# Kernel tuning notes

Measured on AMD Instinct MI355X. Metric: run time of the kernel, lower is better.

Reference implementation:

```python
import jax, jax.numpy as jnp
import numpy as np

DELTA_VAR = 0.5
DELTA_DIST = 1.5
VAR_WEIGHT = 1.0
DIST_WEIGHT = 1.0
REG_WEIGHT = 0.001
K = 16  # number of clusters (labels are in [0, K))


def setup_inputs() -> dict:
    key = jax.random.key(0)
    k1, k2 = jax.random.split(key)
    data = jax.random.normal(k1, (32, 512, 1024), dtype=jnp.float32)
    labels = jax.random.randint(k2, (512, 1024), 0, K, dtype=jnp.int32)
    return {"data": data, "labels": labels}


def reference(data, labels):
    D = data.shape[0]
    pts = data.reshape(D, -1).T          # [N, D] per-pixel embeddings
    lab = labels.reshape(-1)             # [N]

    # Per-cluster size and mean (center). All K clusters are present.
    counts = jax.ops.segment_sum(jnp.ones_like(lab, dtype=pts.dtype), lab,
                                 num_segments=K)          # [K]
    sums = jax.ops.segment_sum(pts, lab, num_segments=K)  # [K, D]
    centers = sums / counts[:, None]                      # [K, D]

    # Variance term: sum over all points of hinge(||center - x|| - dv)^2 / K
    diff = centers[lab] - pts                             # [N, D]
    dist = jnp.sqrt(jnp.sum(diff * diff, axis=-1))        # [N]
    var_term = jnp.sum(jnp.maximum(dist - DELTA_VAR, 0.0) ** 2) / K

    # Distance term: ordered pairs i != j of hinge(2*dd - ||ci - cj||)^2
    cd = centers[:, None, :] - centers[None, :, :]        # [K, K, D]
    sq = jnp.sum(cd * cd, axis=-1)                        # [K, K]
    eye = jnp.eye(K, dtype=bool)
    pd = jnp.sqrt(jnp.where(eye, 1.0, sq))                # safe sqrt on diag
    hinge = jnp.where(eye, 0.0, jnp.maximum(2.0 * DELTA_DIST - pd, 0.0) ** 2)
    dist_term = jnp.sum(hinge) / (K * (K - 1))

    # Regularization term: mean center norm
    reg_term = jnp.sum(jnp.sqrt(jnp.sum(centers * centers, axis=-1))) / K

    return VAR_WEIGHT * var_term + DIST_WEIGHT * dist_term + REG_WEIGHT * reg_term
```

## Files before the change

kernel.cpp:

```cpp
#include <hip/hip_runtime.h>


constexpr int KC = 16;
constexpr int DD = 32;
constexpr int NN = 512 * 1024;
constexpr int N4 = NN / 4;
constexpr int N2 = NN / 2;
constexpr int CHUNKS = 32;
constexpr int GROUPS_PER_CHUNK = N4 / CHUNKS;
constexpr int K1_ITERS = GROUPS_PER_CHUNK / 256;

constexpr int WS_P  = 0;
constexpr int WS_CP = 16384;

__global__ __launch_bounds__(256) void kA_sums(const float4* __restrict__ data4,
                                               const int4* __restrict__ lab4,
                                               float* __restrict__ ws,
                                               float* __restrict__ out) {
    const int tid = threadIdx.x;
    const int chunk = blockIdx.x;
    const int d = blockIdx.y;
    const bool doCnt = (d == 0);

    if (chunk == 0 && d == 0 && tid == 0) out[0] = 0.f;

    __shared__ float acc[KC * 256];
    __shared__ float cnt[KC * 256];
#pragma unroll
    for (int k = 0; k < KC; ++k) acc[k * 256 + tid] = 0.f;
    if (doCnt) {
#pragma unroll
        for (int k = 0; k < KC; ++k) cnt[k * 256 + tid] = 0.f;
    }
    __syncthreads();

    const float4* dplane = data4 + (size_t)d * N4;
    int g = chunk * GROUPS_PER_CHUNK + tid;

    float4 v = dplane[g];
    int4 lb = lab4[g];
    for (int it = 0; it < K1_ITERS; ++it) {
        float4 vn;
        int4 lbn;
        if (it + 1 < K1_ITERS) {
            vn = dplane[g + 256];
            lbn = lab4[g + 256];
        }
        acc[lb.x * 256 + tid] += v.x;
        acc[lb.y * 256 + tid] += v.y;
        acc[lb.z * 256 + tid] += v.z;
        acc[lb.w * 256 + tid] += v.w;
        if (doCnt) {
            cnt[lb.x * 256 + tid] += 1.f;
            cnt[lb.y * 256 + tid] += 1.f;
            cnt[lb.z * 256 + tid] += 1.f;
            cnt[lb.w * 256 + tid] += 1.f;
        }
        v = vn;
        lb = lbn;
        g += 256;
    }
    __syncthreads();

    const int k = tid >> 4, seg = tid & 15;
    float s = 0.f;
#pragma unroll
    for (int i = 0; i < 16; ++i) s += acc[k * 256 + seg * 16 + i];
#pragma unroll
    for (int off = 8; off > 0; off >>= 1) s += __shfl_down(s, off, 16);
    if (seg == 0) ws[WS_P + (k * DD + d) * CHUNKS + chunk] = s;
    if (doCnt) {
        float c = 0.f;
#pragma unroll
        for (int i = 0; i < 16; ++i) c += cnt[k * 256 + seg * 16 + i];
#pragma unroll
        for (int off = 8; off > 0; off >>= 1) c += __shfl_down(c, off, 16);
        if (seg == 0) ws[WS_CP + k * CHUNKS + chunk] = c;
    }
}

__global__ __launch_bounds__(256) void kB_var(const float2* __restrict__ data2,
                                              const int2* __restrict__ lab2,
                                              const float* __restrict__ ws,
                                              float* __restrict__ out) {
    __shared__ float csum[KC * 33];
    __shared__ float ccnt[KC];
    __shared__ float ct2[DD * 32];
    const int tid = threadIdx.x;

    {
        int idx = tid;
        const float* p = ws + WS_P + idx * CHUNKS;
        float s = 0.f;
#pragma unroll
        for (int c = 0; c < CHUNKS; ++c) s += p[c];
        csum[(idx >> 5) * 33 + (idx & 31)] = s;
        idx = tid + 256;
        p = ws + WS_P + idx * CHUNKS;
        s = 0.f;
#pragma unroll
        for (int c = 0; c < CHUNKS; ++c) s += p[c];
        csum[(idx >> 5) * 33 + (idx & 31)] = s;
    }
    if (tid < KC) {
        const float* p = ws + WS_CP + tid * CHUNKS;
        float c = 0.f;
#pragma unroll
        for (int i = 0; i < CHUNKS; ++i) c += p[i];
        ccnt[tid] = c;
    }
    __syncthreads();

    for (int idx = tid; idx < KC * DD; idx += 256) {
        const int k = idx >> 5, d = idx & 31;
        const float c = csum[k * 33 + d] / ccnt[k];
        ct2[d * 32 + k] = c;
        ct2[d * 32 + 16 + k] = c;
    }
    __syncthreads();

    if (blockIdx.x == 0) {
        const int i = tid >> 4, j = tid & 15;
        float val;
        if (i != j) {
            float sq = 0.f;
#pragma unroll
            for (int d = 0; d < DD; ++d) {
                const float df = ct2[d * 32 + i] - ct2[d * 32 + j];
                sq += df * df;
            }
            const float pd = sqrtf(sq);
            const float t = fmaxf(3.0f - pd, 0.f);
            val = t * t * (1.0f / (KC * (KC - 1)));
        } else {
            float s2 = 0.f;
#pragma unroll
            for (int d = 0; d < DD; ++d) s2 += ct2[d * 32 + i] * ct2[d * 32 + i];
            val = sqrtf(s2) * (0.001f / KC);
        }
        __shared__ float red[256];
        red[tid] = val;
        __syncthreads();
        for (int off = 128; off > 0; off >>= 1) {
            if (tid < off) red[tid] += red[tid + off];
            __syncthreads();
        }
        if (tid == 0) atomicAdd(out, red[0]);
        __syncthreads();
    }

    const int g = blockIdx.x * 256 + tid;
    const int2 lb = lab2[g];
    const int dup = (tid & 32) >> 1;
    const int o0 = lb.x + dup, o1 = lb.y + dup;

    float s0 = 0.f, s1 = 0.f;
#pragma unroll 8
    for (int d = 0; d < DD; ++d) {
        const float2 v = data2[(size_t)d * N2 + g];
        const float* ctd = ct2 + d * 32;
        const float d0 = ctd[o0] - v.x; s0 += d0 * d0;
        const float d1 = ctd[o1] - v.y; s1 += d1 * d1;
    }
    const float h0 = fmaxf(sqrtf(s0) - 0.5f, 0.f);
    const float h1 = fmaxf(sqrtf(s1) - 0.5f, 0.f);
    float lsum = h0 * h0 + h1 * h1;

#pragma unroll
    for (int off = 32; off > 0; off >>= 1) lsum += __shfl_down(lsum, off);
    __shared__ float wred[4];
    if ((tid & 63) == 0) wred[tid >> 6] = lsum;
    __syncthreads();
    if (tid == 0) {
        const float s = wred[0] + wred[1] + wred[2] + wred[3];
        atomicAdd(out, s * (1.0f / KC));
    }
}

extern "C" void kernel_launch(void* const* d_in, const int* in_sizes, int n_in,
                              void* d_out, int out_size, void* d_ws, size_t ws_size,
                              hipStream_t stream) {
    const float4* data4 = (const float4*)d_in[0];
    const int4* lab4 = (const int4*)d_in[1];
    float* out = (float*)d_out;
    float* ws = (float*)d_ws;

    kA_sums<<<dim3(CHUNKS, DD), 256, 0, stream>>>(data4, lab4, ws, out);
    kB_var<<<1024, 256, 0, stream>>>((const float2*)d_in[0], (const int2*)d_in[1], ws, out);
}
```

Baseline: 122.6 us.

## Fuse sum and variance passes into one cooperative kernel with grid sync

Merges the per-cluster sum kernel and the variance/distance kernel into a single cooperative launch. A grid-wide sync separates the accumulation phase from the centre-building and variance phase. The chunk count is halved so the grid is 512 blocks, and each thread in the variance pass now handles four pixels with float4 loads instead of two. This removes the second kernel launch and its inter-kernel gap, but it drops to fewer, longer-running blocks and adds the cost of a cooperative launch and a grid barrier.

Result: slower. 254.4 us (+107.5%).

```diff
diff --git a/kernel.cpp b/kernel.cpp
--- a/kernel.cpp
+++ b/kernel.cpp
@@ -1,48 +1,54 @@
 #include <hip/hip_runtime.h>
+#include <hip/hip_cooperative_groups.h>
+
+namespace cg = cooperative_groups;
 
 
 constexpr int KC = 16;
 constexpr int DD = 32;
 constexpr int NN = 512 * 1024;
 constexpr int N4 = NN / 4;
-constexpr int N2 = NN / 2;
-constexpr int CHUNKS = 32;
-constexpr int GROUPS_PER_CHUNK = N4 / CHUNKS;
-constexpr int K1_ITERS = GROUPS_PER_CHUNK / 256;
+constexpr int CHUNKS = 16;
+constexpr int GPC = N4 / CHUNKS;
+constexpr int ITERS = GPC / 256;
+constexpr int NBLK = 512;
 
-constexpr int WS_P  = 0;
-constexpr int WS_CP = 16384;
-
-__global__ __launch_bounds__(256) void kA_sums(const float4* __restrict__ data4,
-                                               const int4* __restrict__ lab4,
-                                               float* __restrict__ ws,
-                                               float* __restrict__ out) {
+__global__ __launch_bounds__(256) void kfused(const float4* __restrict__ data4,
+                                              const int4* __restrict__ lab4,
+                                              float* __restrict__ ws,
+                                              float* __restrict__ out) {
     const int tid = threadIdx.x;
-    const int chunk = blockIdx.x;
-    const int d = blockIdx.y;
+    const int bid = blockIdx.x;
+    const int chunk = bid & 15;
+    const int d = bid >> 4;
     const bool doCnt = (d == 0);
 
-    if (chunk == 0 && d == 0 && tid == 0) out[0] = 0.f;
+    if (bid == 0 && tid == 0) out[0] = 0.f;
 
     __shared__ float acc[KC * 256];
     __shared__ float cnt[KC * 256];
+    __shared__ float csum[512];
+    __shared__ float ccnt[KC];
+    __shared__ float ct2[DD * 32];
+    __shared__ float red[256];
+    __shared__ float wred[4];
+
 #pragma unroll
     for (int k = 0; k < KC; ++k) acc[k * 256 + tid] = 0.f;
     if (doCnt) {
 #pragma unroll
         for (int k = 0; k < KC; ++k) cnt[k * 256 + tid] = 0.f;
     }
-    __syncthreads();
 
     const float4* dplane = data4 + (size_t)d * N4;
-    int g = chunk * GROUPS_PER_CHUNK + tid;
+    int g = chunk * GPC + tid;
 
     float4 v = dplane[g];
     int4 lb = lab4[g];
-    for (int it = 0; it < K1_ITERS; ++it) {
+    for (int it = 0; it < ITERS; ++it) {
         float4 vn;
         int4 lbn;
-        if (it + 1 < K1_ITERS) {
+        if (it + 1 < ITERS) {
             vn = dplane[g + 256];
             lbn = lab4[g + 256];
         }
@@ -62,71 +68,57 @@
     }
     __syncthreads();
 
-    const int k = tid >> 4, seg = tid & 15;
-    float s = 0.f;
+    {
+        const int k = tid >> 4, seg = tid & 15;
+        float s = 0.f;
 #pragma unroll
-    for (int i = 0; i < 16; ++i) s += acc[k * 256 + seg * 16 + i];
+        for (int i = 0; i < 16; ++i) s += acc[k * 256 + seg * 16 + i];
 #pragma unroll
-    for (int off = 8; off > 0; off >>= 1) s += __shfl_down(s, off, 16);
-    if (seg == 0) ws[WS_P + (k * DD + d) * CHUNKS + chunk] = s;
-    if (doCnt) {
+        for (int off = 8; off > 0; off >>= 1) s += __shfl_down(s, off, 16);
+        if (seg == 0) ws[chunk * 512 + k * DD + d] = s;
+        if (doCnt) {
+            float c = 0.f;
+#pragma unroll
+            for (int i = 0; i < 16; ++i) c += cnt[k * 256 + seg * 16 + i];
+#pragma unroll
+            for (int off = 8; off > 0; off >>= 1) c += __shfl_down(c, off, 16);
+            if (seg == 0) ws[8192 + chunk * 16 + k] = c;
+        }
+    }
+
+    __threadfence();
+    cg::this_grid().sync();
+    __threadfence();
+
+    if (tid < KC) {
         float c = 0.f;
 #pragma unroll
-        for (int i = 0; i < 16; ++i) c += cnt[k * 256 + seg * 16 + i];
-#pragma unroll
-        for (int off = 8; off > 0; off >>= 1) c += __shfl_down(c, off, 16);
-        if (seg == 0) ws[WS_CP + k * CHUNKS + chunk] = c;
+        for (int i = 0; i < CHUNKS; ++i) c += ws[8192 + i * 16 + tid];
+        ccnt[tid] = c;
     }
-}
-
-__global__ __launch_bounds__(256) void kB_var(const float2* __restrict__ data2,
-                                              const int2* __restrict__ lab2,
-                                              const float* __restrict__ ws,
-                                              float* __restrict__ out) {
-    __shared__ float csum[KC * 33];
-    __shared__ float ccnt[KC];
-    __shared__ float ct2[DD * 32];
-    const int tid = threadIdx.x;
-
-    {
-        int idx = tid;
-        const float* p = ws + WS_P + idx * CHUNKS;
+    for (int idx = tid; idx < 512; idx += 256) {
         float s = 0.f;
 #pragma unroll
-        for (int c = 0; c < CHUNKS; ++c) s += p[c];
-        csum[(idx >> 5) * 33 + (idx & 31)] = s;
-        idx = tid + 256;
-        p = ws + WS_P + idx * CHUNKS;
-        s = 0.f;
-#pragma unroll
-        for (int c = 0; c < CHUNKS; ++c) s += p[c];
-        csum[(idx >> 5) * 33 + (idx & 31)] = s;
+        for (int cch = 0; cch < CHUNKS; ++cch) s += ws[cch * 512 + idx];
+        csum[idx] = s;
     }
-    if (tid < KC) {
-        const float* p = ws + WS_CP + tid * CHUNKS;
-        float c = 0.f;
-#pragma unroll
-        for (int i = 0; i < CHUNKS; ++i) c += p[i];
-        ccnt[tid] = c;
+    __syncthreads();
+    for (int idx = tid; idx < KC * DD; idx += 256) {
+        const int k = idx >> 5, dd = idx & 31;
+        const float c = csum[k * 32 + dd] / ccnt[k];
+        ct2[dd * 32 + k] = c;
+        ct2[dd * 32 + 16 + k] = c;
     }
     __syncthreads();
 
-    for (int idx = tid; idx < KC * DD; idx += 256) {
-        const int k = idx >> 5, d = idx & 31;
-        const float c = csum[k * 33 + d] / ccnt[k];
-        ct2[d * 32 + k] = c;
-        ct2[d * 32 + 16 + k] = c;
-    }
-    __syncthreads();
-
-    if (blockIdx.x == 0) {
+    if (bid == 0) {
         const int i = tid >> 4, j = tid & 15;
         float val;
         if (i != j) {
             float sq = 0.f;
 #pragma unroll
-            for (int d = 0; d < DD; ++d) {
-                const float df = ct2[d * 32 + i] - ct2[d * 32 + j];
+            for (int dd = 0; dd < DD; ++dd) {
+                const float df = ct2[dd * 32 + i] - ct2[dd * 32 + j];
                 sq += df * df;
             }
             const float pd = sqrtf(sq);
@@ -135,10 +127,9 @@
         } else {
             float s2 = 0.f;
 #pragma unroll
-            for (int d = 0; d < DD; ++d) s2 += ct2[d * 32 + i] * ct2[d * 32 + i];
+            for (int dd = 0; dd < DD; ++dd) s2 += ct2[dd * 32 + i] * ct2[dd * 32 + i];
             val = sqrtf(s2) * (0.001f / KC);
         }
-        __shared__ float red[256];
         red[tid] = val;
         __syncthreads();
         for (int off = 128; off > 0; off >>= 1) {
@@ -146,29 +137,31 @@
             __syncthreads();
         }
         if (tid == 0) atomicAdd(out, red[0]);
-        __syncthreads();
     }
 
-    const int g = blockIdx.x * 256 + tid;
-    const int2 lb = lab2[g];
+    g = bid * 256 + tid;
+    lb = lab4[g];
     const int dup = (tid & 32) >> 1;
-    const int o0 = lb.x + dup, o1 = lb.y + dup;
+    const int o0 = lb.x + dup, o1 = lb.y + dup, o2 = lb.z + dup, o3 = lb.w + dup;
 
-    float s0 = 0.f, s1 = 0.f;
+    float s0 = 0.f, s1 = 0.f, s2 = 0.f, s3 = 0.f;
 #pragma unroll 8
-    for (int d = 0; d < DD; ++d) {
-        const float2 v = data2[(size_t)d * N2 + g];
-        const float* ctd = ct2 + d * 32;
-        const float d0 = ctd[o0] - v.x; s0 += d0 * d0;
-        const float d1 = ctd[o1] - v.y; s1 += d1 * d1;
+    for (int dd = 0; dd < DD; ++dd) {
+        const float4 vv = data4[(size_t)dd * N4 + g];
+        const float* ctd = ct2 + dd * 32;
+        const float d0 = ctd[o0] - vv.x; s0 += d0 * d0;
+        const float d1 = ctd[o1] - vv.y; s1 += d1 * d1;
+        const float d2 = ctd[o2] - vv.z; s2 += d2 * d2;
+        const float d3 = ctd[o3] - vv.w; s3 += d3 * d3;
     }
     const float h0 = fmaxf(sqrtf(s0) - 0.5f, 0.f);
     const float h1 = fmaxf(sqrtf(s1) - 0.5f, 0.f);
-    float lsum = h0 * h0 + h1 * h1;
+    const float h2 = fmaxf(sqrtf(s2) - 0.5f, 0.f);
+    const float h3 = fmaxf(sqrtf(s3) - 0.5f, 0.f);
+    float lsum = h0 * h0 + h1 * h1 + h2 * h2 + h3 * h3;
 
 #pragma unroll
     for (int off = 32; off > 0; off >>= 1) lsum += __shfl_down(lsum, off);
-    __shared__ float wred[4];
     if ((tid & 63) == 0) wred[tid >> 6] = lsum;
     __syncthreads();
     if (tid == 0) {
@@ -185,6 +178,6 @@
     float* out = (float*)d_out;
     float* ws = (float*)d_ws;
 
-    kA_sums<<<dim3(CHUNKS, DD), 256, 0, stream>>>(data4, lab4, ws, out);
-    kB_var<<<1024, 256, 0, stream>>>((const float2*)d_in[0], (const int2*)d_in[1], ws, out);
+    void* args[] = {(void*)&data4, (void*)&lab4, (void*)&ws, (void*)&out};
+    hipLaunchCooperativeKernel((const void*)kfused, dim3(NBLK), dim3(256), args, 0, stream);
 }
```

## Skew shared-memory accumulator columns and widen variance kernel to float4 loads

Applied to the files above, without the earlier changes.

In the sums kernel, each of the four per-thread accumulator updates now targets a column offset by 64, 128 or 192 threads. Loads and stores are split so the four read-modify-writes can issue together, with the aim of reducing LDS bank conflicts and dependency stalls. The variance kernel now handles four pixels per thread with float4/int4 loads and half as many blocks. This cuts the number of blocks that each recompute the centers from the workspace, at the cost of more registers per thread and fewer threads in flight.

Result: faster. 111.9 us (-8.7%).

```diff
diff --git a/kernel.cpp b/kernel.cpp
--- a/kernel.cpp
+++ b/kernel.cpp
@@ -5,7 +5,6 @@
 constexpr int DD = 32;
 constexpr int NN = 512 * 1024;
 constexpr int N4 = NN / 4;
-constexpr int N2 = NN / 2;
 constexpr int CHUNKS = 32;
 constexpr int GROUPS_PER_CHUNK = N4 / CHUNKS;
 constexpr int K1_ITERS = GROUPS_PER_CHUNK / 256;
@@ -34,6 +33,11 @@
     }
     __syncthreads();
 
+    const int c0 = tid;
+    const int c1 = (tid + 64) & 255;
+    const int c2 = (tid + 128) & 255;
+    const int c3 = (tid + 192) & 255;
+
     const float4* dplane = data4 + (size_t)d * N4;
     int g = chunk * GROUPS_PER_CHUNK + tid;
 
@@ -46,15 +50,27 @@
             vn = dplane[g + 256];
             lbn = lab4[g + 256];
         }
-        acc[lb.x * 256 + tid] += v.x;
-        acc[lb.y * 256 + tid] += v.y;
-        acc[lb.z * 256 + tid] += v.z;
-        acc[lb.w * 256 + tid] += v.w;
+        const int i0 = lb.x * 256 + c0;
+        const int i1 = lb.y * 256 + c1;
+        const int i2 = lb.z * 256 + c2;
+        const int i3 = lb.w * 256 + c3;
+        const float a0 = acc[i0];
+        const float a1 = acc[i1];
+        const float a2 = acc[i2];
+        const float a3 = acc[i3];
+        acc[i0] = a0 + v.x;
+        acc[i1] = a1 + v.y;
+        acc[i2] = a2 + v.z;
+        acc[i3] = a3 + v.w;
         if (doCnt) {
-            cnt[lb.x * 256 + tid] += 1.f;
-            cnt[lb.y * 256 + tid] += 1.f;
-            cnt[lb.z * 256 + tid] += 1.f;
-            cnt[lb.w * 256 + tid] += 1.f;
+            const float b0 = cnt[i0];
+            const float b1 = cnt[i1];
+            const float b2 = cnt[i2];
+            const float b3 = cnt[i3];
+            cnt[i0] = b0 + 1.f;
+            cnt[i1] = b1 + 1.f;
+            cnt[i2] = b2 + 1.f;
+            cnt[i3] = b3 + 1.f;
         }
         v = vn;
         lb = lbn;
@@ -79,8 +95,8 @@
     }
 }
 
-__global__ __launch_bounds__(256) void kB_var(const float2* __restrict__ data2,
-                                              const int2* __restrict__ lab2,
+__global__ __launch_bounds__(256) void kB_var(const float4* __restrict__ data4,
+                                              const int4* __restrict__ lab4,
                                               const float* __restrict__ ws,
                                               float* __restrict__ out) {
     __shared__ float csum[KC * 33];
@@ -150,21 +166,25 @@
     }
 
     const int g = blockIdx.x * 256 + tid;
-    const int2 lb = lab2[g];
+    const int4 lb = lab4[g];
     const int dup = (tid & 32) >> 1;
-    const int o0 = lb.x + dup, o1 = lb.y + dup;
-
-    float s0 = 0.f, s1 = 0.f;
+    const int o0 = lb.x + dup, o1 = lb.y + dup, o2 = lb.z + dup, o3 = lb.w + dup;
+
+    float s0 = 0.f, s1 = 0.f, s2 = 0.f, s3 = 0.f;
 #pragma unroll 8
     for (int d = 0; d < DD; ++d) {
-        const float2 v = data2[(size_t)d * N2 + g];
+        const float4 v = data4[(size_t)d * N4 + g];
         const float* ctd = ct2 + d * 32;
         const float d0 = ctd[o0] - v.x; s0 += d0 * d0;
         const float d1 = ctd[o1] - v.y; s1 += d1 * d1;
+        const float d2 = ctd[o2] - v.z; s2 += d2 * d2;
+        const float d3 = ctd[o3] - v.w; s3 += d3 * d3;
     }
     const float h0 = fmaxf(sqrtf(s0) - 0.5f, 0.f);
     const float h1 = fmaxf(sqrtf(s1) - 0.5f, 0.f);
-    float lsum = h0 * h0 + h1 * h1;
+    const float h2 = fmaxf(sqrtf(s2) - 0.5f, 0.f);
+    const float h3 = fmaxf(sqrtf(s3) - 0.5f, 0.f);
+    float lsum = h0 * h0 + h1 * h1 + h2 * h2 + h3 * h3;
 
 #pragma unroll
     for (int off = 32; off > 0; off >>= 1) lsum += __shfl_down(lsum, off);
@@ -186,5 +206,5 @@
     float* ws = (float*)d_ws;
 
     kA_sums<<<dim3(CHUNKS, DD), 256, 0, stream>>>(data4, lab4, ws, out);
-    kB_var<<<1024, 256, 0, stream>>>((const float2*)d_in[0], (const int2*)d_in[1], ws, out);
+    kB_var<<<512, 256, 0, stream>>>(data4, lab4, ws, out);
 }
```
